# Kernel tuning notes

Hardware: AMD Instinct MI355X
Metric: run time of the kernel (lower is better)

Reference implementation:

```python
import jax, jax.numpy as jnp
import numpy as np

B, C_IN, C_OUT, N = 4, 32, 32, 163842


def setup_inputs() -> dict:
    key = jax.random.key(0)
    k1, k2, k3, k4 = jax.random.split(key, 4)
    x = jax.random.normal(k1, (B, C_IN, N), dtype=jnp.float32)
    # nn.Linear(7*in_feats, out_feats): weight [out, 7*in], bias [out]
    W = jax.random.normal(k2, (C_OUT, 7 * C_IN), dtype=jnp.float32) * (1.0 / np.sqrt(7 * C_IN))
    b = jax.random.normal(k3, (C_OUT,), dtype=jnp.float32) * 0.01
    neigh_orders = jax.random.randint(k4, (N, 7), 0, N, dtype=jnp.int32)
    return {"x": x, "W": W, "b": b, "neigh_orders": neigh_orders}


def reference(x, W, b, neigh_orders):
    # x: [B, C_in, N] -> [B, N, C_in]
    xt = jnp.transpose(x, (0, 2, 1))
    # gather 1-ring neighborhood: [B, N, 7, C_in]
    gathered = xt[:, neigh_orders, :]
    Bb, Nn = xt.shape[0], xt.shape[1]
    mat = gathered.reshape(Bb, Nn, 7 * xt.shape[2])  # [B, N, 7*C_in]
    out = jnp.einsum("bnk,ok->bno", mat, W) + b       # [B, N, C_out]
    return jnp.transpose(out, (0, 2, 1))              # [B, C_out, N]
```

## Files before the change

### kernel.cpp

```cpp
#include <hip/hip_runtime.h>
#include <hip/hip_bf16.h>
#include <stdint.h>

#define B_   4
#define CIN  32
#define COUT 32
#define NV   163842
#define K7   7

typedef short bf16x8 __attribute__((ext_vector_type(8)));
typedef float f32x4  __attribute__((ext_vector_type(4)));

__device__ inline uint16_t f2bf(float f) {
    uint32_t u = __float_as_uint(f);
    uint32_t r = (u + 0x7FFFu + ((u >> 16) & 1u)) >> 16;
    return (uint16_t)r;
}

__global__ void k_convw(const float* __restrict__ W, uint16_t* __restrict__ Wb) {
    int i = blockIdx.x * 256 + threadIdx.x;
    if (i < COUT * K7 * CIN) Wb[i] = f2bf(W[i]);
}

__global__ void k_transpose(const float* __restrict__ x, uint16_t* __restrict__ xt) {
    int v = blockIdx.x * 256 + threadIdx.x;
    int b = blockIdx.y;
    if (v >= NV) return;
    const float* xb = x + (size_t)b * CIN * NV;
    uint16_t* row = xt + ((size_t)b * NV + v) * CIN;
    #pragma unroll
    for (int q = 0; q < 4; ++q) {
        bf16x8 pk;
        #pragma unroll
        for (int i = 0; i < 8; ++i) {
            float f = xb[(size_t)(q * 8 + i) * NV + v];
            ((uint16_t*)&pk)[i] = f2bf(f);
        }
        *(bf16x8*)(row + q * 8) = pk;
    }
}

__global__ __launch_bounds__(256) void k_main(const uint16_t* __restrict__ xt,
                                              const uint16_t* __restrict__ Wb,
                                              const float* __restrict__ bias,
                                              const int* __restrict__ neigh,
                                              float* __restrict__ out) {
    const int tid  = threadIdx.x;
    const int lane = tid & 63;
    const int wv   = tid >> 6;
    const int b    = blockIdx.y;
    const int vb   = blockIdx.x * 64 + wv * 16;
    const int l15  = lane & 15;
    const int g    = lane >> 4;
    const int v    = vb + l15;
    const int vv   = (v < NV) ? v : (NV - 1);

    bf16x8 wf[2][K7];
    #pragma unroll
    for (int t = 0; t < 2; ++t)
        #pragma unroll
        for (int j = 0; j < K7; ++j)
            wf[t][j] = *(const bf16x8*)(Wb + (size_t)(t * 16 + l15) * (K7 * CIN) + j * CIN + g * 8);

    int nidx[K7];
    #pragma unroll
    for (int j = 0; j < K7; ++j) nidx[j] = neigh[(size_t)vv * K7 + j];

    const uint16_t* xb = xt + (size_t)b * NV * CIN;
    bf16x8 xf[K7];
    #pragma unroll
    for (int j = 0; j < K7; ++j)
        xf[j] = *(const bf16x8*)(xb + (size_t)nidx[j] * CIN + g * 8);

    f32x4 acc0 = {0.f, 0.f, 0.f, 0.f};
    f32x4 acc1 = {0.f, 0.f, 0.f, 0.f};
    #pragma unroll
    for (int j = 0; j < K7; ++j) {
        acc0 = __builtin_amdgcn_mfma_f32_16x16x32_bf16(wf[0][j], xf[j], acc0, 0, 0, 0);
        acc1 = __builtin_amdgcn_mfma_f32_16x16x32_bf16(wf[1][j], xf[j], acc1, 0, 0, 0);
    }

    if (v < NV) {
        float* ob = out + (size_t)b * COUT * NV + v;
        #pragma unroll
        for (int r = 0; r < 4; ++r) {
            int o0 = g * 4 + r;
            ob[(size_t)o0 * NV] = acc0[r] + bias[o0];
            int o1 = 16 + g * 4 + r;
            ob[(size_t)o1 * NV] = acc1[r] + bias[o1];
        }
    }
}

extern "C" void kernel_launch(void* const* d_in, const int* in_sizes, int n_in,
                              void* d_out, int out_size, void* d_ws, size_t ws_size,
                              hipStream_t stream) {
    const float* x     = (const float*)d_in[0];
    const float* W     = (const float*)d_in[1];
    const float* bias  = (const float*)d_in[2];
    const int*   neigh = (const int*)d_in[3];
    float* out = (float*)d_out;

    uint16_t* xt = (uint16_t*)d_ws;
    uint16_t* Wb = xt + (size_t)B_ * NV * CIN;

    k_convw<<<(COUT * K7 * CIN + 255) / 256, 256, 0, stream>>>(W, Wb);

    dim3 g1((NV + 255) / 256, B_);
    k_transpose<<<g1, 256, 0, stream>>>(x, xt);

    dim3 g2((NV + 63) / 64, B_);
    k_main<<<g2, 256, 0, stream>>>(xt, Wb, bias, neigh, out);
}
```

Before: 254.2 us.

## Interleave batch into vertex rows and process all batches per block

Changes the transposed bf16 buffer layout from [B][N][C] to [N][B][C], so one neighbor gather fetches a contiguous 256-byte row holding all four batches. The main kernel now loops over batches inside each wave, so neighbor indices and weight fragments are loaded once per vertex rather than once per batch, and the grid drops the batch dimension. Gathers become larger and more contiguous, at the cost of more accumulator registers per thread and fewer blocks.

```diff
diff --git a/kernel.cpp b/kernel.cpp
--- a/kernel.cpp
+++ b/kernel.cpp
@@ -27,7 +27,7 @@
     int b = blockIdx.y;
     if (v >= NV) return;
     const float* xb = x + (size_t)b * CIN * NV;
-    uint16_t* row = xt + ((size_t)b * NV + v) * CIN;
+    uint16_t* row = xt + (size_t)v * (B_ * CIN) + b * CIN;
     #pragma unroll
     for (int q = 0; q < 4; ++q) {
         bf16x8 pk;
@@ -48,7 +48,6 @@
     const int tid  = threadIdx.x;
     const int lane = tid & 63;
     const int wv   = tid >> 6;
-    const int b    = blockIdx.y;
     const int vb   = blockIdx.x * 64 + wv * 16;
     const int l15  = lane & 15;
     const int g    = lane >> 4;
@@ -66,28 +65,40 @@
     #pragma unroll
     for (int j = 0; j < K7; ++j) nidx[j] = neigh[(size_t)vv * K7 + j];
 
-    const uint16_t* xb = xt + (size_t)b * NV * CIN;
-    bf16x8 xf[K7];
+    f32x4 acc[B_][2];
     #pragma unroll
-    for (int j = 0; j < K7; ++j)
-        xf[j] = *(const bf16x8*)(xb + (size_t)nidx[j] * CIN + g * 8);
+    for (int b = 0; b < B_; ++b) {
+        acc[b][0] = (f32x4){0.f, 0.f, 0.f, 0.f};
+        acc[b][1] = (f32x4){0.f, 0.f, 0.f, 0.f};
+    }
 
-    f32x4 acc0 = {0.f, 0.f, 0.f, 0.f};
-    f32x4 acc1 = {0.f, 0.f, 0.f, 0.f};
     #pragma unroll
     for (int j = 0; j < K7; ++j) {
-        acc0 = __builtin_amdgcn_mfma_f32_16x16x32_bf16(wf[0][j], xf[j], acc0, 0, 0, 0);
-        acc1 = __builtin_amdgcn_mfma_f32_16x16x32_bf16(wf[1][j], xf[j], acc1, 0, 0, 0);
+        const uint16_t* row = xt + (size_t)nidx[j] * (B_ * CIN);
+        bf16x8 xf[B_];
+        #pragma unroll
+        for (int b = 0; b < B_; ++b)
+            xf[b] = *(const bf16x8*)(row + b * CIN + g * 8);
+        #pragma unroll
+        for (int b = 0; b < B_; ++b) {
+            acc[b][0] = __builtin_amdgcn_mfma_f32_16x16x32_bf16(wf[0][j], xf[b], acc[b][0], 0, 0, 0);
+            acc[b][1] = __builtin_amdgcn_mfma_f32_16x16x32_bf16(wf[1][j], xf[b], acc[b][1], 0, 0, 0);
+        }
     }
 
     if (v < NV) {
-        float* ob = out + (size_t)b * COUT * NV + v;
+        f32x4 bia0 = *(const f32x4*)(bias + g * 4);
+        f32x4 bia1 = *(const f32x4*)(bias + 16 + g * 4);
         #pragma unroll
-        for (int r = 0; r < 4; ++r) {
-            int o0 = g * 4 + r;
-            ob[(size_t)o0 * NV] = acc0[r] + bias[o0];
-            int o1 = 16 + g * 4 + r;
-            ob[(size_t)o1 * NV] = acc1[r] + bias[o1];
+        for (int b = 0; b < B_; ++b) {
+            float* ob = out + (size_t)b * COUT * NV + v;
+            #pragma unroll
+            for (int r = 0; r < 4; ++r) {
+                int o0 = g * 4 + r;
+                ob[(size_t)o0 * NV] = acc[b][0][r] + bia0[r];
+                int o1 = 16 + g * 4 + r;
+                ob[(size_t)o1 * NV] = acc[b][1][r] + bia1[r];
+            }
         }
     }
 }
@@ -102,13 +113,13 @@
     float* out = (float*)d_out;
 
     uint16_t* xt = (uint16_t*)d_ws;
-    uint16_t* Wb = xt + (size_t)B_ * NV * CIN;
+    uint16_t* Wb = xt + (size_t)NV * B_ * CIN;
 
     k_convw<<<(COUT * K7 * CIN + 255) / 256, 256, 0, stream>>>(W, Wb);
 
     dim3 g1((NV + 255) / 256, B_);
     k_transpose<<<g1, 256, 0, stream>>>(x, xt);
 
-    dim3 g2((NV + 63) / 64, B_);
+    dim3 g2((NV + 63) / 64, 1);
     k_main<<<g2, 256, 0, stream>>>(xt, Wb, bias, neigh, out);
 }
```

Measured after the change: 244.2 us. 1.04x faster.
